# Kernel tuning notes

Measured on AMD Instinct MI355X. Metric: run time of the kernel, lower is better.

The kernel has to match this reference:

```python
import jax, jax.numpy as jnp
import numpy as np

N = 100000      # nodes
E = 800000      # edges (before self-loops)
G = 128         # graphs
IN = 64         # per-table embedding dim (6 tables -> 384 input features)
L = 128         # layer_embd
OUT = 128       # out_embd
H = 2           # attention heads (concat=False -> mean over heads)
VOCABS = [33, 5, 3, 4, 2, 3]
NEG_SLOPE = 0.2
BN_EPS = 1e-5


def _seg_softmax(logits, seg, n):
    # softmax of per-edge/per-node logits grouped by segment id
    m = jax.ops.segment_max(logits, seg, num_segments=n)
    e = jnp.exp(logits - m[seg])
    s = jax.ops.segment_sum(e, seg, num_segments=n)
    return e / (s[seg] + 1e-16)


def _gat_conv(x, W, a_src, a_dst, b, src, dst, n):
    # PyG GATConv, add_self_loops already applied to (src,dst), concat=False
    h = (x @ W).reshape(n, H, -1)                 # [N,H,C]
    al_s = jnp.sum(h * a_src, axis=-1)            # [N,H]
    al_d = jnp.sum(h * a_dst, axis=-1)            # [N,H]
    e = jax.nn.leaky_relu(al_s[src] + al_d[dst], NEG_SLOPE)   # [E,H]
    alpha = _seg_softmax(e, dst, n)               # softmax over each dst's in-edges
    msg = h[src] * alpha[:, :, None]              # [E,H,C]
    out = jax.ops.segment_sum(msg, dst, num_segments=n)       # [N,H,C]
    return out.mean(axis=1) + b                   # head-mean + bias


def setup_inputs() -> dict:
    key = jax.random.key(0)
    ks = jax.random.split(key, 40)
    cols = [jax.random.randint(ks[i], (N, 1), 0, VOCABS[i]) for i in range(6)]
    x = jnp.concatenate(cols, axis=1).astype(jnp.int64)
    edge_index = jax.random.randint(ks[6], (2, E), 0, N).astype(jnp.int64)
    edge_type = jax.random.randint(ks[7], (E,), 0, 4).astype(jnp.int64)
    batch = jnp.sort(jax.random.randint(ks[8], (N,), 0, G)).astype(jnp.int64)
    s = 0.05
    p = {}
    for i in range(6):
        p[f"emb{i}"] = jax.random.normal(ks[10 + i], (VOCABS[i], IN)) * s
    p["W1"] = jax.random.normal(ks[16], (6 * IN, H * L)) * s
    p["as1"] = jax.random.normal(ks[17], (H, L)) * s
    p["ad1"] = jax.random.normal(ks[18], (H, L)) * s
    p["b1"] = jnp.zeros((L,))
    p["W2"] = jax.random.normal(ks[19], (L, H * OUT)) * s
    p["as2"] = jax.random.normal(ks[20], (H, OUT)) * s
    p["ad2"] = jax.random.normal(ks[21], (H, OUT)) * s
    p["b2"] = jnp.zeros((OUT,))
    p["gw1"] = jax.random.normal(ks[22], (OUT, OUT)) * s
    p["gb1"] = jnp.zeros((OUT,))
    p["bn_g"] = jnp.ones((OUT,))
    p["bn_b"] = jnp.zeros((OUT,))
    p["bn_m"] = jnp.zeros((OUT,))
    p["bn_v"] = jnp.ones((OUT,))
    p["gw2"] = jax.random.normal(ks[23], (OUT, 1)) * s
    p["gb2"] = jnp.zeros((1,))
    p["glw"] = jax.random.normal(ks[24], (OUT, 1)) * s
    p["glb"] = jnp.zeros((1,))
    return dict(x=x, edge_index=edge_index, edge_type=edge_type, batch=batch, **p)


def reference(x, edge_index, edge_type, batch,
              emb0, emb1, emb2, emb3, emb4, emb5,
              W1, as1, ad1, b1, W2, as2, ad2, b2,
              gw1, gb1, bn_g, bn_b, bn_m, bn_v, gw2, gb2, glw, glb):
    n = x.shape[0]
    embs = [emb0, emb1, emb2, emb3, emb4, emb5]
    x_ = jnp.concatenate([embs[i][x[:, i]] for i in range(6)], axis=1)  # [N, 6*IN]
    loops = jnp.arange(n)
    src = jnp.concatenate([edge_index[0], loops])
    dst = jnp.concatenate([edge_index[1], loops])
    out = jax.nn.sigmoid(_gat_conv(x_, W1, as1, ad1, b1, src, dst, n))
    out = jax.nn.sigmoid(_gat_conv(out, W2, as2, ad2, b2, src, dst, n))
    # GlobalAttention pooling (eval-mode BatchNorm in gate_nn)
    gh = out @ gw1 + gb1
    gh = (gh - bn_m) / jnp.sqrt(bn_v + BN_EPS) * bn_g + bn_b
    gh = jax.nn.relu(gh)
    logits = gh @ gw2 + gb2                       # [N,1]
    gate = _seg_softmax(logits, batch, G)         # softmax over nodes per graph
    pooled = jax.ops.segment_sum(gate * out, batch, num_segments=G)  # [G,OUT]
    return jax.nn.sigmoid(pooled @ glw + glb)     # [G,1]
```

## Files before the change

### kernel.cpp

```cpp
#include <hip/hip_runtime.h>
#include <hip/hip_bf16.h>
#include <hip/hip_fp16.h>

#define NN 100000
#define EE 800000
#define GG 128

typedef short bf16x8 __attribute__((ext_vector_type(8)));
typedef float f32x4 __attribute__((ext_vector_type(4)));
typedef float f32x2 __attribute__((ext_vector_type(2)));

__device__ __forceinline__ float bf2f(unsigned short v) {
    union { unsigned int u; float f; } x; x.u = ((unsigned int)v) << 16; return x.f;
}
__device__ __forceinline__ unsigned short f2bf(float f) {
    union { float f; unsigned int u; } x; x.f = f;
    unsigned int r = x.u + 0x7fffu + ((x.u >> 16) & 1u);
    return (unsigned short)(r >> 16);
}
__device__ __forceinline__ float sigmoidf_(float x) { return 1.f / (1.f + __expf(-x)); }
__device__ __forceinline__ float ldp(const void* p, int i, int f) {
    return f ? ((const float*)p)[i] : bf2f(((const unsigned short*)p)[i]);
}

#if defined(__has_builtin)
#if __has_builtin(__builtin_amdgcn_cvt_pk_f32_fp8) && __has_builtin(__builtin_amdgcn_cvt_pk_fp8_f32)
#define USE_HW_FP8 1
#endif
#endif
#ifndef USE_HW_FP8
#define USE_HW_FP8 0
#endif

#if USE_HW_FP8
__device__ __forceinline__ int fp8_pack2(float a, float b) {
    return __builtin_amdgcn_cvt_pk_fp8_f32(a, b, 0, false);
}
__device__ __forceinline__ void fp8_dec4v(unsigned int q, f32x2& lo, f32x2& hi) {
    lo = __builtin_amdgcn_cvt_pk_f32_fp8((int)q, false);
    hi = __builtin_amdgcn_cvt_pk_f32_fp8((int)q, true);
}
#else
__device__ __forceinline__ unsigned char f2bf8(float f) {
    unsigned short u = __half_as_ushort(__float2half(f));
    unsigned short r = u + 0x7f + ((u >> 8) & 1);
    return (unsigned char)(r >> 8);
}
__device__ __forceinline__ int fp8_pack2(float a, float b) {
    return (int)f2bf8(a) | ((int)f2bf8(b) << 8);
}
__device__ __forceinline__ float bf8_dec(unsigned int b) {
    return __half2float(__ushort_as_half((unsigned short)(b << 8)));
}
__device__ __forceinline__ void fp8_dec4v(unsigned int q, f32x2& lo, f32x2& hi) {
    lo[0] = bf8_dec(q & 0xff); lo[1] = bf8_dec((q >> 8) & 0xff);
    hi[0] = bf8_dec((q >> 16) & 0xff); hi[1] = bf8_dec(q >> 24);
}
#endif

__global__ void k_probe2(const unsigned int* __restrict__ w, const int* __restrict__ ei,
                         int* __restrict__ fflag, int* __restrict__ iflag) {
    __shared__ int s[256];
    int t = threadIdx.x;
    if (blockIdx.x == 0) {
        int cnt = 0;
        for (int i = t; i < 1024; i += 256) {
            unsigned int v = w[i];
            int e = (v >> 7) & 0xff;
            cnt += (e >= 100 && e <= 127) ? 1 : 0;
        }
        s[t] = cnt; __syncthreads();
        for (int d = 128; d > 0; d >>= 1) { if (t < d) s[t] += s[t + d]; __syncthreads(); }
        if (t == 0) fflag[0] = (s[0] >= 512) ? 0 : 1;
    } else {
        int nz = 0;
        for (int i = t; i < 1024; i += 256) nz |= ei[2 * i + 1];
        s[t] = nz; __syncthreads();
        for (int d = 128; d > 0; d >>= 1) { if (t < d) s[t] |= s[t + d]; __syncthreads(); }
        if (t == 0) iflag[0] = (s[0] == 0) ? 1 : 0;
    }
}

__global__ void k_hist(const int* __restrict__ ei, const int* __restrict__ iflag,
                       int* __restrict__ count) {
    int e = blockIdx.x * 256 + threadIdx.x;
    if (e < EE) {
        int f = iflag[0];
        int d = ei[(EE + e) << f];
        atomicAdd(&count[d], 1);
    }
}

__global__ void k_chunk_sum(const int* __restrict__ count, int* __restrict__ csum) {
    __shared__ int s[256];
    int t = threadIdx.x;
    int base = blockIdx.x * 1024 + t * 4;
    int acc = 0;
    #pragma unroll
    for (int j = 0; j < 4; j++) { int n = base + j; if (n < NN) acc += count[n]; }
    s[t] = acc; __syncthreads();
    for (int d = 128; d > 0; d >>= 1) { if (t < d) s[t] += s[t + d]; __syncthreads(); }
    if (t == 0) csum[blockIdx.x] = s[0];
}

__global__ void k_chunk_scan(const int* __restrict__ csum, int* __restrict__ coff, int nchunk) {
    __shared__ int s[256];
    int t = threadIdx.x;
    int v = (t < nchunk) ? csum[t] : 0;
    s[t] = v; __syncthreads();
    for (int d = 1; d < 256; d <<= 1) {
        int x = (t >= d) ? s[t - d] : 0;
        __syncthreads(); s[t] += x; __syncthreads();
    }
    if (t < nchunk) coff[t] = s[t] - v;
}

__global__ void k_scan_write(const int* __restrict__ count, const int* __restrict__ coff,
                             int* __restrict__ offset, int* __restrict__ cursor) {
    __shared__ int s[256];
    int t = threadIdx.x;
    int base = blockIdx.x * 1024 + t * 4;
    int v[4]; int acc = 0;
    #pragma unroll
    for (int j = 0; j < 4; j++) { v[j] = (base + j < NN) ? count[base + j] : 0; acc += v[j]; }
    s[t] = acc; __syncthreads();
    for (int d = 1; d < 256; d <<= 1) {
        int x = (t >= d) ? s[t - d] : 0;
        __syncthreads(); s[t] += x; __syncthreads();
    }
    int pre = s[t] - acc + coff[blockIdx.x];
    #pragma unroll
    for (int j = 0; j < 4; j++) {
        if (base + j < NN) { offset[base + j] = pre; cursor[base + j] = pre; pre += v[j]; }
    }
}

__global__ void k_scatter(const int* __restrict__ ei, const int* __restrict__ iflag,
                          int* __restrict__ cursor, int* __restrict__ sorted) {
    int e = blockIdx.x * 256 + threadIdx.x;
    if (e < EE) {
        int f = iflag[0];
        int s = ei[e << f];
        int d = ei[(EE + e) << f];
        int p = atomicAdd(&cursor[d], 1);
        sorted[p] = s;
    }
}

__constant__ int c_vbase[7] = {0, 33, 38, 41, 45, 47, 50};
__global__ __launch_bounds__(256) void k_prep(
    const void* e0, const void* e1, const void* e2,
    const void* e3, const void* e4, const void* e5,
    const void* W1, const void* W2,
    const void* as1, const void* ad1, const void* b1,
    const void* as2, const void* ad2, const void* b2,
    const void* gw1, const void* gb1,
    const void* bng, const void* bnb, const void* bnm, const void* bnv,
    const void* gw2, const void* gb2, const void* glw, const void* glb,
    const int* __restrict__ fflag,
    unsigned short* __restrict__ W2T,
    unsigned short* __restrict__ GWT, float* __restrict__ gb1p,
    float* __restrict__ vs1, float* __restrict__ vd1,
    float* __restrict__ vs2, float* __restrict__ vd2,
    float* __restrict__ vb1, float* __restrict__ vb2,
    float* __restrict__ gw2f, float* __restrict__ glwf,
    float* __restrict__ gb2f, float* __restrict__ glbf,
    float* __restrict__ P) {
    int f = fflag[0];
    if (blockIdx.x >= 128) {
        int r = blockIdx.x - 128;
        int c = threadIdx.x;
        int t = 0;
        while (r >= c_vbase[t + 1]) t++;
        int v = r - c_vbase[t];
        const void* emb = (t == 0) ? e0 : (t == 1) ? e1 : (t == 2) ? e2 :
                          (t == 3) ? e3 : (t == 4) ? e4 : e5;
        float acc = 0.f;
        #pragma unroll 8
        for (int k = 0; k < 64; k++) {
            acc += ldp(emb, v * 64 + k, f) * ldp(W1, (t * 64 + k) * 256 + c, f);
        }
        P[r * 256 + c] = acc;
        return;
    }
    int i = blockIdx.x * 256 + threadIdx.x;
    if (i < 32768) { int k = i / 256, n = i % 256; W2T[n * 128 + k] = f2bf(ldp(W2, i, f)); }
    if (i < 16384) {
        int n = i >> 7, k = i & 127;
        float sc = ldp(bng, n, f) * rsqrtf(ldp(bnv, n, f) + 1e-5f);
        GWT[i] = f2bf(ldp(gw1, k * 128 + n, f) * sc);
    }
    if (i < 256) {
        vs1[i] = ldp(as1, i, f); vd1[i] = ldp(ad1, i, f);
        vs2[i] = ldp(as2, i, f); vd2[i] = ldp(ad2, i, f);
    }
    if (i < 128) {
        vb1[i] = ldp(b1, i, f); vb2[i] = ldp(b2, i, f);
        gw2f[i] = ldp(gw2, i, f); glwf[i] = ldp(glw, i, f);
        float sc = ldp(bng, i, f) * rsqrtf(ldp(bnv, i, f) + 1e-5f);
        gb1p[i] = (ldp(gb1, i, f) - ldp(bnm, i, f)) * sc + ldp(bnb, i, f);
    }
    if (i == 0) { gb2f[0] = ldp(gb2, 0, f); glbf[0] = ldp(glb, 0, f); }
}

__global__ __launch_bounds__(256) void k_embsum(
    const int* __restrict__ x_raw, const int* __restrict__ iflag,
    const float* __restrict__ P,
    const float* __restrict__ avs, const float* __restrict__ avd,
    unsigned char* __restrict__ H8,
    float* __restrict__ alS, float* __restrict__ alD) {
    int node = blockIdx.x * 4 + (threadIdx.x >> 6);
    if (node >= NN) return;
    int f = iflag[0];
    int lane = threadIdx.x & 63;
    int c0 = lane * 4;
    int ix[6];
    #pragma unroll
    for (int t = 0; t < 6; t++) ix[t] = (c_vbase[t] + x_raw[(node * 6 + t) << f]) * 256 + c0;
    float4 a = *(const float4*)(P + ix[0]);
    #pragma unroll
    for (int t = 1; t < 6; t++) {
        float4 b = *(const float4*)(P + ix[t]);
        a.x += b.x; a.y += b.y; a.z += b.z; a.w += b.w;
    }
    float4 sv = *(const float4*)(avs + c0);
    float4 dv = *(const float4*)(avd + c0);
    float ps = a.x * sv.x + a.y * sv.y + a.z * sv.z + a.w * sv.w;
    float pd = a.x * dv.x + a.y * dv.y + a.z * dv.z + a.w * dv.w;
    #pragma unroll
    for (int m = 1; m < 32; m <<= 1) {
        ps += __shfl_xor(ps, m);
        pd += __shfl_xor(pd, m);
    }
    if ((lane & 31) == 0) {
        int head = lane >> 5;
        alS[node * 2 + head] = ps;
        alD[node * 2 + head] = pd;
    }
    unsigned int u = ((unsigned)fp8_pack2(a.x, a.y) & 0xffffu) |
                     ((unsigned)fp8_pack2(a.z, a.w) << 16);
    *(unsigned int*)(H8 + (size_t)node * 256 + c0) = u;
}

__global__ __launch_bounds__(256, 2) void k_gemm(
    const unsigned short* __restrict__ Ain,
    const unsigned short* __restrict__ WT, unsigned char* __restrict__ H8,
    const float* __restrict__ avs, const float* __restrict__ avd,
    float* __restrict__ alS, float* __restrict__ alD,
    int K)
{
    __shared__ __align__(16) unsigned short As[64 * 32];
    __shared__ __align__(16) unsigned short Bs[256 * 32];
    int tid = threadIdx.x;
    int wave = tid >> 6, lane = tid & 63;
    int quad = lane >> 4, lr = lane & 15;
    int m0 = blockIdx.x * 64;

    f32x4 zero4 = {0.f, 0.f, 0.f, 0.f};
    f32x4 acc[16];
    #pragma unroll
    for (int j = 0; j < 16; j++) acc[j] = zero4;

    for (int k0 = 0; k0 < K; k0 += 32) {
        {
            int row = tid >> 2, part = tid & 3;
            int gr = m0 + row; if (gr >= NN) gr = NN - 1;
            int g = ((row >> 4) << 6) + (part << 4) + (row & 15);
            g ^= (part << 1);
            *(uint4*)(&As[g * 8]) = *(const uint4*)(Ain + (size_t)gr * K + k0 + part * 8);
        }
        #pragma unroll
        for (int i = 0; i < 4; i++) {
            int idx = tid + i * 256;
            int row = idx >> 2, part = idx & 3;
            int g = ((row >> 4) << 6) + (part << 4) + (row & 15);
            g ^= (part << 1);
            *(uint4*)(&Bs[g * 8]) =
                *(const uint4*)(WT + (size_t)row * K + k0 + part * 8);
        }
        __syncthreads();

        int sw = (quad << 1);
        bf16x8 af0 = *(const bf16x8*)(&As[((wave * 64 + lane) ^ sw) * 8]);
        #pragma unroll
        for (int ni = 0; ni < 16; ni++) {
            bf16x8 bfv = *(const bf16x8*)(&Bs[((ni * 64 + lane) ^ sw) * 8]);
            acc[ni] = __builtin_amdgcn_mfma_f32_16x16x32_bf16(af0, bfv, acc[ni], 0, 0, 0);
        }
        __syncthreads();
    }

    float svv[16], dvv[16];
    #pragma unroll
    for (int ni = 0; ni < 16; ni++) { svv[ni] = avs[ni * 16 + lr]; dvv[ni] = avd[ni * 16 + lr]; }
    #pragma unroll
    for (int r = 0; r < 4; r++) {
        int grow = m0 + wave * 16 + quad * 4 + r;
        float ps0 = 0.f, ps1 = 0.f, pd0 = 0.f, pd1 = 0.f;
        if (grow < NN) {
            #pragma unroll
            for (int ni = 0; ni < 16; ni += 2) {
                float v0 = acc[ni][r], v1 = acc[ni + 1][r];
                int pk = fp8_pack2(v0, v1);
                H8[(size_t)grow * 256 + ni * 16 + lr] = (unsigned char)(pk & 0xff);
                H8[(size_t)grow * 256 + (ni + 1) * 16 + lr] = (unsigned char)((pk >> 8) & 0xff);
                if (ni < 8) { ps0 += v0 * svv[ni] + v1 * svv[ni + 1]; pd0 += v0 * dvv[ni] + v1 * dvv[ni + 1]; }
                else        { ps1 += v0 * svv[ni] + v1 * svv[ni + 1]; pd1 += v0 * dvv[ni] + v1 * dvv[ni + 1]; }
            }
        }
        #pragma unroll
        for (int m = 1; m < 16; m <<= 1) {
            ps0 += __shfl_xor(ps0, m); ps1 += __shfl_xor(ps1, m);
            pd0 += __shfl_xor(pd0, m); pd1 += __shfl_xor(pd1, m);
        }
        if (lr == 0 && grow < NN) {
            alS[grow * 2 + 0] = ps0; alS[grow * 2 + 1] = ps1;
            alD[grow * 2 + 0] = pd0; alD[grow * 2 + 1] = pd1;
        }
    }
}

__device__ __forceinline__ float edge_w(float e) {
    e = e > 0.f ? e : 0.2f * e;
    e = fminf(fmaxf(e, -60.f), 60.f);
    return __expf(e);
}
__global__ __launch_bounds__(256) void k_agg(const unsigned char* __restrict__ H8,
                                             const float* __restrict__ alS, const float* __restrict__ alD,
                                             const int* __restrict__ sorted, const int* __restrict__ offs,
                                             const int* __restrict__ cnts,
                                             const float* __restrict__ bias,
                                             unsigned short* __restrict__ Out) {
    __shared__ uint4 lw[4][64];
    int wid = threadIdx.x >> 6;
    int node = blockIdx.x * 4 + wid;
    if (node >= NN) return;
    int lane = threadIdx.x & 63;
    int head = lane >> 5;
    float2 adv = *(const float2*)(alD + node * 2);
    float myAd = head ? adv.y : adv.x;
    const unsigned char* Hl = H8 + lane * 4;

    float ws = edge_w(alS[node * 2 + head] + myAd);
    unsigned int qv = *(const unsigned int*)(Hl + ((unsigned)node << 8));
    f32x2 lo, hi; fp8_dec4v(qv, lo, hi);
    float den = ws;
    f32x2 wsv = {ws, ws};
    f32x2 n01 = lo * wsv, n23 = hi * wsv;

    int off = offs[node], cnt = cnts[node];
    for (int c = 0; c < cnt; c += 64) {
        int m = cnt - c; if (m > 64) m = 64;
        int j = off + c + (lane < m ? lane : 0);
        int s = sorted[j];
        float2 asv = *(const float2*)(alS + s * 2);
        float w0 = edge_w(asv.x + adv.x);
        float w1 = edge_w(asv.y + adv.y);
        lw[wid][lane] = make_uint4((unsigned)s << 8, __float_as_uint(w0), __float_as_uint(w1), 0u);
        int i = 0;
        for (; i + 8 <= m; i += 8) {
            uint4 e[8];
            #pragma unroll
            for (int u = 0; u < 8; u++) e[u] = lw[wid][i + u];
            unsigned q[8];
            #pragma unroll
            for (int u = 0; u < 8; u++) q[u] = *(const unsigned int*)(Hl + e[u].x);
            #pragma unroll
            for (int u = 0; u < 8; u++) {
                float w = __uint_as_float(head ? e[u].z : e[u].y);
                f32x2 l, h; fp8_dec4v(q[u], l, h);
                den += w;
                f32x2 wv = {w, w};
                n01 += l * wv;
                n23 += h * wv;
            }
        }
        for (; i + 4 <= m; i += 4) {
            uint4 e[4];
            #pragma unroll
            for (int u = 0; u < 4; u++) e[u] = lw[wid][i + u];
            unsigned q[4];
            #pragma unroll
            for (int u = 0; u < 4; u++) q[u] = *(const unsigned int*)(Hl + e[u].x);
            #pragma unroll
            for (int u = 0; u < 4; u++) {
                float w = __uint_as_float(head ? e[u].z : e[u].y);
                f32x2 l, h; fp8_dec4v(q[u], l, h);
                den += w;
                f32x2 wv = {w, w};
                n01 += l * wv;
                n23 += h * wv;
            }
        }
        for (; i < m; i++) {
            uint4 e0 = lw[wid][i];
            unsigned q0 = *(const unsigned int*)(Hl + e0.x);
            float w = __uint_as_float(head ? e0.z : e0.y);
            f32x2 l, h; fp8_dec4v(q0, l, h);
            den += w;
            f32x2 wv = {w, w};
            n01 += l * wv;
            n23 += h * wv;
        }
    }
    float inv = 1.f / den;
    float v0 = n01[0] * inv, v1 = n01[1] * inv, v2 = n23[0] * inv, v3 = n23[1] * inv;
    float o0 = 0.5f * (v0 + __shfl_xor(v0, 32));
    float o1 = 0.5f * (v1 + __shfl_xor(v1, 32));
    float o2 = 0.5f * (v2 + __shfl_xor(v2, 32));
    float o3 = 0.5f * (v3 + __shfl_xor(v3, 32));
    if (lane < 32) {
        int c = lane * 4;
        float4 bv = *(const float4*)(bias + c);
        o0 = sigmoidf_(o0 + bv.x);
        o1 = sigmoidf_(o1 + bv.y);
        o2 = sigmoidf_(o2 + bv.z);
        o3 = sigmoidf_(o3 + bv.w);
        uint2 pv;
        pv.x = (unsigned int)f2bf(o0) | ((unsigned int)f2bf(o1) << 16);
        pv.y = (unsigned int)f2bf(o2) | ((unsigned int)f2bf(o3) << 16);
        *(uint2*)(Out + (size_t)node * 128 + c) = pv;
    }
}

__global__ __launch_bounds__(256, 2) void k_gate(
    const unsigned short* __restrict__ Obuf,
    const unsigned short* __restrict__ GWT,
    const float* __restrict__ gb1p, const float* __restrict__ gw2f,
    const float* __restrict__ gb2f,
    const int* __restrict__ batch_raw, const int* __restrict__ iflag,
    float* __restrict__ accv, float* __restrict__ accw)
{
    __shared__ __align__(16) unsigned short As[64 * 128];
    __shared__ __align__(16) unsigned short Bs[128 * 128];
    __shared__ float wlds[64];
    __shared__ int gid[64];
    int tid = threadIdx.x;
    int wave = tid >> 6, lane = tid & 63;
    int quad = lane >> 4, lr = lane & 15;
    int m0 = blockIdx.x * 64;

    #pragma unroll
    for (int i = 0; i < 4; i++) {
        int idx = tid + i * 256;
        int row = idx >> 4, p = idx & 15;
        int gr = m0 + row; if (gr >= NN) gr = NN - 1;
        int slot = row * 16 + (p & 8) + ((p & 7) ^ (row & 7));
        *(uint4*)(&As[slot * 8]) = *(const uint4*)(Obuf + (size_t)gr * 128 + p * 8);
    }
    #pragma unroll
    for (int i = 0; i < 8; i++) {
        int idx = tid + i * 256;
        int row = idx >> 4, p = idx & 15;
        int slot = row * 16 + (p & 8) + ((p & 7) ^ (row & 7));
        *(uint4*)(&Bs[slot * 8]) = *(const uint4*)(GWT + (size_t)row * 128 + p * 8);
    }
    if (tid < 64) {
        int nd = m0 + tid; if (nd >= NN) nd = NN - 1;
        gid[tid] = batch_raw[nd << iflag[0]];
    }
    __syncthreads();

    f32x4 zero4 = {0.f, 0.f, 0.f, 0.f};
    f32x4 acc[8];
    #pragma unroll
    for (int j = 0; j < 8; j++) acc[j] = zero4;

    int rowa = wave * 16 + lr;
    #pragma unroll
    for (int k0 = 0; k0 < 128; k0 += 32) {
        int kb = k0 >> 3;
        int pa = (kb & 8) + (((kb & 7) + quad) ^ (lr & 7));
        bf16x8 af0 = *(const bf16x8*)(&As[(rowa * 16 + pa) * 8]);
        #pragma unroll
        for (int ni = 0; ni < 8; ni++) {
            int rowb = ni * 16 + lr;
            bf16x8 bfv = *(const bf16x8*)(&Bs[(rowb * 16 + pa) * 8]);
            acc[ni] = __builtin_amdgcn_mfma_f32_16x16x32_bf16(af0, bfv, acc[ni], 0, 0, 0);
        }
    }

    float gb[8], gw[8];
    #pragma unroll
    for (int ni = 0; ni < 8; ni++) { gb[ni] = gb1p[ni * 16 + lr]; gw[ni] = gw2f[ni * 16 + lr]; }
    #pragma unroll
    for (int r = 0; r < 4; r++) {
        int row = wave * 16 + quad * 4 + r;
        float part = 0.f;
        #pragma unroll
        for (int ni = 0; ni < 8; ni++) {
            float v = acc[ni][r] + gb[ni];
            v = v > 0.f ? v : 0.f;
            part += v * gw[ni];
        }
        #pragma unroll
        for (int m = 1; m < 16; m <<= 1) part += __shfl_xor(part, m);
        if (lr == 0) {
            float w = (m0 + row < NN) ? __expf(part + gb2f[0]) : 0.f;
            wlds[row] = w;
        }
    }
    __syncthreads();

    int ch = tid & 127;
    int r0 = (tid >> 7) * 32;
    int p = ch >> 3, ip = ch & 7;
    float accum = 0.f, aw = 0.f;
    int g = -1;
    for (int rr = 0; rr < 32; rr++) {
        int row = r0 + rr;
        int gi = gid[row];
        float w = wlds[row];
        if (gi != g) {
            if (g >= 0) {
                atomicAdd(&accv[g * 128 + ch], accum);
                if (ch == 0) atomicAdd(&accw[g], aw);
            }
            g = gi; accum = 0.f; aw = 0.f;
        }
        int slot = row * 16 + (p & 8) + ((p & 7) ^ (row & 7));
        float val = bf2f(As[slot * 8 + ip]);
        accum += w * val;
        if (ch == 0) aw += w;
    }
    if (g >= 0) {
        atomicAdd(&accv[g * 128 + ch], accum);
        if (ch == 0) atomicAdd(&accw[g], aw);
    }
}

__global__ __launch_bounds__(128) void k_pfin(const float* __restrict__ accv,
                                              const float* __restrict__ accw,
                                              const float* __restrict__ glwf,
                                              const float* __restrict__ glbf,
                                              const int* __restrict__ fflag,
                                              void* __restrict__ out) {
    __shared__ float sv[128];
    int g = blockIdx.x, t = threadIdx.x;
    float pooled = accv[g * 128 + t] / (accw[g] + 1e-16f);
    sv[t] = pooled * glwf[t];
    __syncthreads();
    for (int s = 64; s > 0; s >>= 1) { if (t < s) sv[t] += sv[t + s]; __syncthreads(); }
    if (t == 0) {
        float r = sigmoidf_(sv[0] + glbf[0]);
        if (fflag[0]) ((float*)out)[g] = r;
        else ((unsigned short*)out)[g] = f2bf(r);
    }
}

extern "C" void kernel_launch(void* const* d_in, const int* in_sizes, int n_in,
                              void* d_out, int out_size, void* d_ws, size_t ws_size,
                              hipStream_t stream) {
    const int* x_raw  = (const int*)d_in[0];
    const int* ei_raw = (const int*)d_in[1];
    const int* b_raw  = (const int*)d_in[3];

    char* p = (char*)d_ws;
    auto alloc = [&](size_t bytes) { void* r = (void*)p; p += (bytes + 255) & ~(size_t)255; return r; };
    unsigned char* H8   = (unsigned char*)alloc((size_t)NN * 256);
    unsigned short* Obuf = (unsigned short*)alloc((size_t)NN * 128 * 2);
    float* alS   = (float*)alloc((size_t)NN * 2 * 4);
    float* alD   = (float*)alloc((size_t)NN * 2 * 4);
    char* z0 = p;
    int* count   = (int*)alloc((size_t)NN * 4);
    float* accv  = (float*)alloc(GG * 128 * 4);
    float* accw  = (float*)alloc(GG * 4);
    size_t zlen = (size_t)(p - z0);
    int* offs    = (int*)alloc((size_t)NN * 4);
    int* cursor  = (int*)alloc((size_t)NN * 4);
    int* sorted  = (int*)alloc((size_t)EE * 4);
    int* csum    = (int*)alloc(256 * 4);
    int* coff    = (int*)alloc(256 * 4);
    unsigned short* W2T  = (unsigned short*)alloc(256 * 128 * 2);
    unsigned short* GWT  = (unsigned short*)alloc(128 * 128 * 2);
    float* gb1p = (float*)alloc(128 * 4);
    float* Ptab = (float*)alloc(50 * 256 * 4);
    int* iflag  = (int*)alloc(256);
    int* fflag  = (int*)alloc(256);
    float* vs1  = (float*)alloc(256 * 4);
    float* vd1  = (float*)alloc(256 * 4);
    float* vs2  = (float*)alloc(256 * 4);
    float* vd2  = (float*)alloc(256 * 4);
    float* vb1  = (float*)alloc(128 * 4);
    float* vb2  = (float*)alloc(128 * 4);
    float* gw2f = (float*)alloc(128 * 4);
    float* glwf = (float*)alloc(128 * 4);
    float* gb2f = (float*)alloc(4);
    float* glbf = (float*)alloc(4);

    const int NCHUNK = (NN + 1023) / 1024;
    const int NBM = (NN + 63) / 64;
    const int NBE = (EE + 255) / 256;
    const int NB4 = (NN + 3) / 4;

    hipMemsetAsync(z0, 0, zlen, stream);

    k_probe2<<<2, 256, 0, stream>>>((const unsigned int*)d_in[10], ei_raw, fflag, iflag);
    k_hist<<<NBE, 256, 0, stream>>>(ei_raw, iflag, count);
    k_prep<<<178, 256, 0, stream>>>(
        d_in[4], d_in[5], d_in[6], d_in[7], d_in[8], d_in[9],
        d_in[10], d_in[14],
        d_in[11], d_in[12], d_in[13], d_in[15], d_in[16], d_in[17],
        d_in[18], d_in[19], d_in[20], d_in[21], d_in[22], d_in[23],
        d_in[24], d_in[25], d_in[26], d_in[27],
        fflag, W2T, GWT, gb1p,
        vs1, vd1, vs2, vd2, vb1, vb2, gw2f, glwf, gb2f, glbf, Ptab);

    k_chunk_sum<<<NCHUNK, 256, 0, stream>>>(count, csum);
    k_chunk_scan<<<1, 256, 0, stream>>>(csum, coff, NCHUNK);
    k_scan_write<<<NCHUNK, 256, 0, stream>>>(count, coff, offs, cursor);
    k_scatter<<<NBE, 256, 0, stream>>>(ei_raw, iflag, cursor, sorted);

    k_embsum<<<NB4, 256, 0, stream>>>(x_raw, iflag, Ptab, vs1, vd1, H8, alS, alD);
    k_agg<<<NB4, 256, 0, stream>>>(H8, alS, alD, sorted, offs, count, vb1, Obuf);

    k_gemm<<<NBM, 256, 0, stream>>>(Obuf, W2T, H8, vs2, vd2, alS, alD, 128);
    k_agg<<<NB4, 256, 0, stream>>>(H8, alS, alD, sorted, offs, count, vb2, Obuf);

    k_gate<<<NBM, 256, 0, stream>>>(Obuf, GWT, gb1p, gw2f, gb2f, b_raw, iflag, accv, accw);
    k_pfin<<<GG, 128, 0, stream>>>(accv, accw, glwf, glbf, fflag, d_out);
}
```

Before: 413.3 us.

## Merge probe, histogram and prep into one launch; merge scatter with embsum

Folds the dtype/index-width probes, the edge histogram and the parameter preparation into a single k_front kernel. Every histogram block now recomputes the index-width probe redundantly, and the prep blocks compute the float-format flag locally. Edge scatter and the embedding-sum kernel also become one k_mid launch, since they are independent and can share the GPU. This removes three kernel launches and the serial gaps between them, at the cost of redundant probe reads in every histogram block.

```diff
diff --git a/kernel.cpp b/kernel.cpp
--- a/kernel.cpp
+++ b/kernel.cpp
@@ -5,6 +5,9 @@
 #define NN 100000
 #define EE 800000
 #define GG 128
+#define NBE 3125
+#define NPREP 178
+#define NB4 25000
 
 typedef short bf16x8 __attribute__((ext_vector_type(8)));
 typedef float f32x4 __attribute__((ext_vector_type(4)));
@@ -58,11 +61,47 @@
 }
 #endif
 
-__global__ void k_probe2(const unsigned int* __restrict__ w, const int* __restrict__ ei,
-                         int* __restrict__ fflag, int* __restrict__ iflag) {
+__constant__ int c_vbase[7] = {0, 33, 38, 41, 45, 47, 50};
+
+__global__ __launch_bounds__(256) void k_front(
+    const int* __restrict__ ei, int* __restrict__ count,
+    int* __restrict__ iflag, int* __restrict__ fflag,
+    const void* e0, const void* e1, const void* e2,
+    const void* e3, const void* e4, const void* e5,
+    const void* W1, const void* W2,
+    const void* as1, const void* ad1, const void* b1,
+    const void* as2, const void* ad2, const void* b2,
+    const void* gw1, const void* gb1,
+    const void* bng, const void* bnb, const void* bnm, const void* bnv,
+    const void* gw2, const void* gb2, const void* glw, const void* glb,
+    unsigned short* __restrict__ W2T,
+    unsigned short* __restrict__ GWT, float* __restrict__ gb1p,
+    float* __restrict__ vs1, float* __restrict__ vd1,
+    float* __restrict__ vs2, float* __restrict__ vd2,
+    float* __restrict__ vb1, float* __restrict__ vb2,
+    float* __restrict__ gw2f, float* __restrict__ glwf,
+    float* __restrict__ gb2f, float* __restrict__ glbf,
+    float* __restrict__ P)
+{
     __shared__ int s[256];
     int t = threadIdx.x;
-    if (blockIdx.x == 0) {
+    int b = blockIdx.x;
+    if (b < NBE) {
+        int nz = 0;
+        for (int i = t; i < 1024; i += 256) nz |= ei[2 * i + 1];
+        s[t] = nz; __syncthreads();
+        for (int d = 128; d > 0; d >>= 1) { if (t < d) s[t] |= s[t + d]; __syncthreads(); }
+        int f = (s[0] == 0) ? 1 : 0;
+        if (b == 0 && t == 0) iflag[0] = f;
+        int e = b * 256 + t;
+        if (e < EE) {
+            int d = ei[(EE + e) << f];
+            atomicAdd(&count[d], 1);
+        }
+        return;
+    }
+    {
+        const unsigned int* w = (const unsigned int*)W1;
         int cnt = 0;
         for (int i = t; i < 1024; i += 256) {
             unsigned int v = w[i];
@@ -71,24 +110,44 @@
         }
         s[t] = cnt; __syncthreads();
         for (int d = 128; d > 0; d >>= 1) { if (t < d) s[t] += s[t + d]; __syncthreads(); }
-        if (t == 0) fflag[0] = (s[0] >= 512) ? 0 : 1;
-    } else {
-        int nz = 0;
-        for (int i = t; i < 1024; i += 256) nz |= ei[2 * i + 1];
-        s[t] = nz; __syncthreads();
-        for (int d = 128; d > 0; d >>= 1) { if (t < d) s[t] |= s[t + d]; __syncthreads(); }
-        if (t == 0) iflag[0] = (s[0] == 0) ? 1 : 0;
-    }
-}
-
-__global__ void k_hist(const int* __restrict__ ei, const int* __restrict__ iflag,
-                       int* __restrict__ count) {
-    int e = blockIdx.x * 256 + threadIdx.x;
-    if (e < EE) {
-        int f = iflag[0];
-        int d = ei[(EE + e) << f];
-        atomicAdd(&count[d], 1);
-    }
+    }
+    int f = (s[0] >= 512) ? 0 : 1;
+    int pb = b - NBE;
+    if (pb == 0 && t == 0) fflag[0] = f;
+    if (pb >= 128) {
+        int r = pb - 128;
+        int c = t;
+        int tb = 0;
+        while (r >= c_vbase[tb + 1]) tb++;
+        int v = r - c_vbase[tb];
+        const void* emb = (tb == 0) ? e0 : (tb == 1) ? e1 : (tb == 2) ? e2 :
+                          (tb == 3) ? e3 : (tb == 4) ? e4 : e5;
+        float acc = 0.f;
+        #pragma unroll 8
+        for (int k = 0; k < 64; k++) {
+            acc += ldp(emb, v * 64 + k, f) * ldp(W1, (tb * 64 + k) * 256 + c, f);
+        }
+        P[r * 256 + c] = acc;
+        return;
+    }
+    int i = pb * 256 + t;
+    if (i < 32768) { int k = i / 256, n = i % 256; W2T[n * 128 + k] = f2bf(ldp(W2, i, f)); }
+    if (i < 16384) {
+        int n = i >> 7, k = i & 127;
+        float sc = ldp(bng, n, f) * rsqrtf(ldp(bnv, n, f) + 1e-5f);
+        GWT[i] = f2bf(ldp(gw1, k * 128 + n, f) * sc);
+    }
+    if (i < 256) {
+        vs1[i] = ldp(as1, i, f); vd1[i] = ldp(ad1, i, f);
+        vs2[i] = ldp(as2, i, f); vd2[i] = ldp(ad2, i, f);
+    }
+    if (i < 128) {
+        vb1[i] = ldp(b1, i, f); vb2[i] = ldp(b2, i, f);
+        gw2f[i] = ldp(gw2, i, f); glwf[i] = ldp(glw, i, f);
+        float sc = ldp(bng, i, f) * rsqrtf(ldp(bnv, i, f) + 1e-5f);
+        gb1p[i] = (ldp(gb1, i, f) - ldp(bnm, i, f)) * sc + ldp(bnb, i, f);
+    }
+    if (i == 0) { gb2f[0] = ldp(gb2, 0, f); glbf[0] = ldp(glb, 0, f); }
 }
 
 __global__ void k_chunk_sum(const int* __restrict__ count, int* __restrict__ csum) {
@@ -135,83 +194,29 @@
     }
 }
 
-__global__ void k_scatter(const int* __restrict__ ei, const int* __restrict__ iflag,
-                          int* __restrict__ cursor, int* __restrict__ sorted) {
-    int e = blockIdx.x * 256 + threadIdx.x;
-    if (e < EE) {
-        int f = iflag[0];
-        int s = ei[e << f];
-        int d = ei[(EE + e) << f];
-        int p = atomicAdd(&cursor[d], 1);
-        sorted[p] = s;
-    }
-}
-
-__constant__ int c_vbase[7] = {0, 33, 38, 41, 45, 47, 50};
-__global__ __launch_bounds__(256) void k_prep(
-    const void* e0, const void* e1, const void* e2,
-    const void* e3, const void* e4, const void* e5,
-    const void* W1, const void* W2,
-    const void* as1, const void* ad1, const void* b1,
-    const void* as2, const void* ad2, const void* b2,
-    const void* gw1, const void* gb1,
-    const void* bng, const void* bnb, const void* bnm, const void* bnv,
-    const void* gw2, const void* gb2, const void* glw, const void* glb,
-    const int* __restrict__ fflag,
-    unsigned short* __restrict__ W2T,
-    unsigned short* __restrict__ GWT, float* __restrict__ gb1p,
-    float* __restrict__ vs1, float* __restrict__ vd1,
-    float* __restrict__ vs2, float* __restrict__ vd2,
-    float* __restrict__ vb1, float* __restrict__ vb2,
-    float* __restrict__ gw2f, float* __restrict__ glwf,
-    float* __restrict__ gb2f, float* __restrict__ glbf,
-    float* __restrict__ P) {
-    int f = fflag[0];
-    if (blockIdx.x >= 128) {
-        int r = blockIdx.x - 128;
-        int c = threadIdx.x;
-        int t = 0;
-        while (r >= c_vbase[t + 1]) t++;
-        int v = r - c_vbase[t];
-        const void* emb = (t == 0) ? e0 : (t == 1) ? e1 : (t == 2) ? e2 :
-                          (t == 3) ? e3 : (t == 4) ? e4 : e5;
-        float acc = 0.f;
-        #pragma unroll 8
-        for (int k = 0; k < 64; k++) {
-            acc += ldp(emb, v * 64 + k, f) * ldp(W1, (t * 64 + k) * 256 + c, f);
-        }
-        P[r * 256 + c] = acc;
-        return;
-    }
-    int i = blockIdx.x * 256 + threadIdx.x;
-    if (i < 32768) { int k = i / 256, n = i % 256; W2T[n * 128 + k] = f2bf(ldp(W2, i, f)); }
-    if (i < 16384) {
-        int n = i >> 7, k = i & 127;
-        float sc = ldp(bng, n, f) * rsqrtf(ldp(bnv, n, f) + 1e-5f);
-        GWT[i] = f2bf(ldp(gw1, k * 128 + n, f) * sc);
-    }
-    if (i < 256) {
-        vs1[i] = ldp(as1, i, f); vd1[i] = ldp(ad1, i, f);
-        vs2[i] = ldp(as2, i, f); vd2[i] = ldp(ad2, i, f);
-    }
-    if (i < 128) {
-        vb1[i] = ldp(b1, i, f); vb2[i] = ldp(b2, i, f);
-        gw2f[i] = ldp(gw2, i, f); glwf[i] = ldp(glw, i, f);
-        float sc = ldp(bng, i, f) * rsqrtf(ldp(bnv, i, f) + 1e-5f);
-        gb1p[i] = (ldp(gb1, i, f) - ldp(bnm, i, f)) * sc + ldp(bnb, i, f);
-    }
-    if (i == 0) { gb2f[0] = ldp(gb2, 0, f); glbf[0] = ldp(glb, 0, f); }
-}
-
-__global__ __launch_bounds__(256) void k_embsum(
-    const int* __restrict__ x_raw, const int* __restrict__ iflag,
+__global__ __launch_bounds__(256) void k_mid(
+    const int* __restrict__ ei, const int* __restrict__ x_raw,
+    const int* __restrict__ iflag,
+    int* __restrict__ cursor, int* __restrict__ sorted,
     const float* __restrict__ P,
     const float* __restrict__ avs, const float* __restrict__ avd,
     unsigned char* __restrict__ H8,
-    float* __restrict__ alS, float* __restrict__ alD) {
-    int node = blockIdx.x * 4 + (threadIdx.x >> 6);
+    float* __restrict__ alS, float* __restrict__ alD)
+{
+    int b = blockIdx.x;
+    int f = iflag[0];
+    if (b < NBE) {
+        int e = b * 256 + threadIdx.x;
+        if (e < EE) {
+            int s = ei[e << f];
+            int d = ei[(EE + e) << f];
+            int p = atomicAdd(&cursor[d], 1);
+            sorted[p] = s;
+        }
+        return;
+    }
+    int node = (b - NBE) * 4 + (threadIdx.x >> 6);
     if (node >= NN) return;
-    int f = iflag[0];
     int lane = threadIdx.x & 63;
     int c0 = lane * 4;
     int ix[6];
@@ -220,8 +225,8 @@
     float4 a = *(const float4*)(P + ix[0]);
     #pragma unroll
     for (int t = 1; t < 6; t++) {
-        float4 b = *(const float4*)(P + ix[t]);
-        a.x += b.x; a.y += b.y; a.z += b.z; a.w += b.w;
+        float4 bb = *(const float4*)(P + ix[t]);
+        a.x += bb.x; a.y += bb.y; a.z += bb.z; a.w += bb.w;
     }
     float4 sv = *(const float4*)(avs + c0);
     float4 dv = *(const float4*)(avd + c0);
@@ -590,28 +595,26 @@
 
     const int NCHUNK = (NN + 1023) / 1024;
     const int NBM = (NN + 63) / 64;
-    const int NBE = (EE + 255) / 256;
-    const int NB4 = (NN + 3) / 4;
 
     hipMemsetAsync(z0, 0, zlen, stream);
 
-    k_probe2<<<2, 256, 0, stream>>>((const unsigned int*)d_in[10], ei_raw, fflag, iflag);
-    k_hist<<<NBE, 256, 0, stream>>>(ei_raw, iflag, count);
-    k_prep<<<178, 256, 0, stream>>>(
+    k_front<<<NBE + NPREP, 256, 0, stream>>>(
+        ei_raw, count, iflag, fflag,
         d_in[4], d_in[5], d_in[6], d_in[7], d_in[8], d_in[9],
         d_in[10], d_in[14],
         d_in[11], d_in[12], d_in[13], d_in[15], d_in[16], d_in[17],
         d_in[18], d_in[19], d_in[20], d_in[21], d_in[22], d_in[23],
         d_in[24], d_in[25], d_in[26], d_in[27],
-        fflag, W2T, GWT, gb1p,
+        W2T, GWT, gb1p,
         vs1, vd1, vs2, vd2, vb1, vb2, gw2f, glwf, gb2f, glbf, Ptab);
 
     k_chunk_sum<<<NCHUNK, 256, 0, stream>>>(count, csum);
     k_chunk_scan<<<1, 256, 0, stream>>>(csum, coff, NCHUNK);
     k_scan_write<<<NCHUNK, 256, 0, stream>>>(count, coff, offs, cursor);
-    k_scatter<<<NBE, 256, 0, stream>>>(ei_raw, iflag, cursor, sorted);
-
-    k_embsum<<<NB4, 256, 0, stream>>>(x_raw, iflag, Ptab, vs1, vd1, H8, alS, alD);
+
+    k_mid<<<NBE + NB4, 256, 0, stream>>>(ei_raw, x_raw, iflag, cursor, sorted,
+                                         Ptab, vs1, vd1, H8, alS, alD);
+
     k_agg<<<NB4, 256, 0, stream>>>(H8, alS, alD, sorted, offs, count, vb1, Obuf);
 
     k_gemm<<<NBM, 256, 0, stream>>>(Obuf, W2T, H8, vs2, vd2, alS, alD, 128);
```

Result: no change. 406.0 us (median of 2 runs) (-1.8%).
